# Optimization experiments

Hardware: AMD Instinct MI355X
Metric: run time of the kernel (lower is better)

Reference implementation:

```python
import jax, jax.numpy as jnp
import numpy as np

NUM_HEADS = 32
NUM_KV_HEADS = 8
HEAD_DIM = 128
SCALE = 0.08838834764831845  # 1/sqrt(128)
BATCH = 16
NUM_BLOCKS = 4096
BLOCK_SIZE = 16
BLOCKS_PER_SEQ = 256
MAX_SEQ = BLOCKS_PER_SEQ * BLOCK_SIZE  # 4096


def setup_inputs() -> dict:
    key = jax.random.key(0)
    ks = jax.random.split(key, 8)
    q = jax.random.normal(ks[0], (BATCH, NUM_HEADS, HEAD_DIM), dtype=jnp.float32)
    k = jax.random.normal(ks[1], (BATCH, NUM_KV_HEADS, HEAD_DIM), dtype=jnp.float32)
    v = jax.random.normal(ks[2], (BATCH, NUM_KV_HEADS, HEAD_DIM), dtype=jnp.float32)
    k_cache = jax.random.normal(ks[3], (NUM_BLOCKS, BLOCK_SIZE, NUM_KV_HEADS, HEAD_DIM), dtype=jnp.float32)
    v_cache = jax.random.normal(ks[4], (NUM_BLOCKS, BLOCK_SIZE, NUM_KV_HEADS, HEAD_DIM), dtype=jnp.float32)
    block_tables = jax.random.randint(ks[5], (BATCH, BLOCKS_PER_SEQ), 0, NUM_BLOCKS, dtype=jnp.int32)
    context_lens = jax.random.randint(ks[6], (BATCH,), 1, MAX_SEQ, dtype=jnp.int32)
    slot_mapping = jax.random.randint(ks[7], (BATCH,), 0, NUM_BLOCKS * BLOCK_SIZE, dtype=jnp.int32)
    return {"q": q, "k": k, "v": v, "k_cache": k_cache, "v_cache": v_cache,
            "block_tables": block_tables, "context_lens": context_lens,
            "slot_mapping": slot_mapping}


def reference(q, k, v, k_cache, v_cache, block_tables, context_lens, slot_mapping):
    B = q.shape[0]
    n_rep = NUM_HEADS // NUM_KV_HEADS

    # store_kvcache: scatter new K/V tokens into the flat-slot view of the cache
    kc = k_cache.reshape(-1, NUM_KV_HEADS, HEAD_DIM).at[slot_mapping].set(k)
    vc = v_cache.reshape(-1, NUM_KV_HEADS, HEAD_DIM).at[slot_mapping].set(v)
    kc = kc.reshape(k_cache.shape)
    vc = vc.reshape(v_cache.shape)

    # paged gather: [B, nb, bs, KV, D] -> [B, S, KV, D]
    k_seq = kc[block_tables].reshape(B, -1, NUM_KV_HEADS, HEAD_DIM)
    v_seq = vc[block_tables].reshape(B, -1, NUM_KV_HEADS, HEAD_DIM)
    S = k_seq.shape[1]

    # GQA: group query heads instead of materializing repeat_kv (same math)
    qg = q.reshape(B, NUM_KV_HEADS, n_rep, HEAD_DIM)
    scores = jnp.einsum('bgrd,bsgd->bgrs', qg, k_seq) * SCALE  # [B, KV, n_rep, S]

    valid = jnp.arange(S, dtype=jnp.int32)[None, :] < context_lens[:, None]  # [B, S]
    scores = jnp.where(valid[:, None, None, :], scores, -jnp.inf)
    p = jax.nn.softmax(scores, axis=-1)

    o = jnp.einsum('bgrs,bsgd->bgrd', p, v_seq)  # [B, KV, n_rep, D]
    return o.reshape(B, NUM_HEADS, HEAD_DIM)
```

## Files before the change

### kernel.cpp

```cpp
#include <hip/hip_runtime.h>
#include <math.h>

#define BATCH 16
#define NH 32
#define KVH 8
#define NREP 4
#define HD 128
#define BS 16
#define BPS 256
#define MAXSEQ 4096
#define CHUNK 512
#define CBLK (CHUNK / BS)
#define ATT_SCALE 0.08838834764831845f
#define REC (NREP * HD + 2 * NREP)

__global__ __launch_bounds__(256) void kv_scatter(
    const float* __restrict__ k, const float* __restrict__ v,
    const int* __restrict__ slot_mapping,
    float* __restrict__ k_cache, float* __restrict__ v_cache) {
  int b = blockIdx.x;
  int slot = slot_mapping[b];
  size_t base = (size_t)slot * (KVH * HD);
  for (int i = threadIdx.x; i < KVH * HD; i += 256) {
    k_cache[base + i] = k[b * KVH * HD + i];
    v_cache[base + i] = v[b * KVH * HD + i];
  }
}

__global__ __launch_bounds__(256) void attn_decode(
    const float* __restrict__ q,
    const float* __restrict__ k_cache,
    const float* __restrict__ v_cache,
    const int* __restrict__ block_tables,
    const int* __restrict__ context_lens,
    float* __restrict__ part,
    float* __restrict__ out,
    int nsplits) {
  const int split = blockIdx.x;
  const int kvh   = blockIdx.y;
  const int b     = blockIdx.z;
  const int tid   = threadIdx.x;
  const int ctx   = context_lens[b];
  const int span  = MAXSEQ / nsplits;
  const int s_begin = split * span;

  float* rec = part + (((size_t)b * KVH + kvh) * nsplits + split) * REC;

  if (s_begin >= ctx) {
    if (nsplits > 1 && tid < NREP) {
      rec[NREP * HD + tid] = -INFINITY;
      rec[NREP * HD + NREP + tid] = 0.f;
    }
    return;
  }
  const int s_end = min(ctx, s_begin + span);

  __shared__ float sc[NREP][CHUNK];
  __shared__ int   btab[CBLK];
  __shared__ float red[8][NREP * HD];
  __shared__ float m_sh[NREP], l_sh[NREP], alpha_sh[NREP];

  const int wave = tid >> 6;
  const int lane = tid & 63;
  const int half = lane >> 5;
  const int l32  = lane & 31;
  const int grp  = tid >> 5;
  const int gl   = tid & 31;

  float4 q4[NREP];
#pragma unroll
  for (int h = 0; h < NREP; ++h)
    q4[h] = *(const float4*)(q + ((size_t)b * NH + kvh * NREP + h) * HD + l32 * 4);

  if (tid < NREP) { m_sh[tid] = -INFINITY; l_sh[tid] = 0.f; }

  float acc[NREP][4];
#pragma unroll
  for (int h = 0; h < NREP; ++h)
#pragma unroll
    for (int j = 0; j < 4; ++j) acc[h][j] = 0.f;

  for (int c0 = s_begin; c0 < s_end; c0 += CHUNK) {
    const int n_tok = min(s_end - c0, CHUNK);

    __syncthreads();
    if (tid < CBLK) {
      int bi = (c0 >> 4) + tid;
      btab[tid] = (bi < BPS) ? block_tables[b * BPS + bi] : 0;
    }
    __syncthreads();

    for (int t = wave * 2 + half; t < n_tok; t += 8) {
      int blk = btab[t >> 4];
      const float4 kk = *(const float4*)(
          k_cache + ((size_t)blk * BS + (t & 15)) * (KVH * HD) + kvh * HD + l32 * 4);
      float p0 = kk.x * q4[0].x + kk.y * q4[0].y + kk.z * q4[0].z + kk.w * q4[0].w;
      float p1 = kk.x * q4[1].x + kk.y * q4[1].y + kk.z * q4[1].z + kk.w * q4[1].w;
      float p2 = kk.x * q4[2].x + kk.y * q4[2].y + kk.z * q4[2].z + kk.w * q4[2].w;
      float p3 = kk.x * q4[3].x + kk.y * q4[3].y + kk.z * q4[3].z + kk.w * q4[3].w;
#pragma unroll
      for (int off = 1; off < 32; off <<= 1) {
        p0 += __shfl_xor(p0, off);
        p1 += __shfl_xor(p1, off);
        p2 += __shfl_xor(p2, off);
        p3 += __shfl_xor(p3, off);
      }
      if (l32 == 0) {
        sc[0][t] = p0 * ATT_SCALE;
        sc[1][t] = p1 * ATT_SCALE;
        sc[2][t] = p2 * ATT_SCALE;
        sc[3][t] = p3 * ATT_SCALE;
      }
    }
    __syncthreads();

    {
      const int h = wave;
      float mloc = -INFINITY;
      for (int t = lane; t < n_tok; t += 64) mloc = fmaxf(mloc, sc[h][t]);
#pragma unroll
      for (int off = 1; off < 64; off <<= 1) mloc = fmaxf(mloc, __shfl_xor(mloc, off));
      float m_old = m_sh[h];
      float m_new = fmaxf(m_old, mloc);
      float sum = 0.f;
      for (int t = lane; t < n_tok; t += 64) {
        float e = __expf(sc[h][t] - m_new);
        sc[h][t] = e;
        sum += e;
      }
#pragma unroll
      for (int off = 1; off < 64; off <<= 1) sum += __shfl_xor(sum, off);
      if (lane == 0) {
        float alpha = (m_old == -INFINITY) ? 0.f : __expf(m_old - m_new);
        alpha_sh[h] = alpha;
        l_sh[h] = l_sh[h] * alpha + sum;
        m_sh[h] = m_new;
      }
    }
    __syncthreads();

    {
      float a[NREP] = {alpha_sh[0], alpha_sh[1], alpha_sh[2], alpha_sh[3]};
#pragma unroll
      for (int h = 0; h < NREP; ++h)
#pragma unroll
        for (int j = 0; j < 4; ++j) acc[h][j] *= a[h];
      for (int t = grp; t < n_tok; t += 8) {
        int blk = btab[t >> 4];
        const float4 vv = *(const float4*)(
            v_cache + ((size_t)blk * BS + (t & 15)) * (KVH * HD) + kvh * HD + gl * 4);
#pragma unroll
        for (int h = 0; h < NREP; ++h) {
          float pp = sc[h][t];
          acc[h][0] += pp * vv.x;
          acc[h][1] += pp * vv.y;
          acc[h][2] += pp * vv.z;
          acc[h][3] += pp * vv.w;
        }
      }
    }
  }

#pragma unroll
  for (int h = 0; h < NREP; ++h)
#pragma unroll
    for (int j = 0; j < 4; ++j) red[grp][h * HD + gl * 4 + j] = acc[h][j];
  __syncthreads();

  for (int o = tid; o < NREP * HD; o += 256) {
    float s = 0.f;
#pragma unroll
    for (int g = 0; g < 8; ++g) s += red[g][o];
    int h = o >> 7, d = o & 127;
    if (nsplits == 1) {
      out[((size_t)b * NH + kvh * NREP + h) * HD + d] = s / l_sh[h];
    } else {
      rec[o] = s;
    }
  }
  if (nsplits > 1 && tid < NREP) {
    rec[NREP * HD + tid] = m_sh[tid];
    rec[NREP * HD + NREP + tid] = l_sh[tid];
  }
}

__global__ __launch_bounds__(256) void attn_combine(
    const float* __restrict__ part, float* __restrict__ out, int nsplits) {
  const int kvh = blockIdx.x;
  const int b   = blockIdx.y;
  const int tid = threadIdx.x;
  const float* base = part + ((size_t)b * KVH + kvh) * nsplits * REC;

  __shared__ float w_sh[8][NREP];
  __shared__ float L_sh[NREP];

  if (tid < NREP) {
    const int h = tid;
    float M = -INFINITY;
    for (int s = 0; s < nsplits; ++s)
      M = fmaxf(M, base[s * REC + NREP * HD + h]);
    float L = 0.f;
    for (int s = 0; s < nsplits; ++s) {
      float m = base[s * REC + NREP * HD + h];
      float l = base[s * REC + NREP * HD + NREP + h];
      float w = (l > 0.f) ? __expf(m - M) : 0.f;
      w_sh[s][h] = w;
      L += l * w;
    }
    L_sh[h] = L;
  }
  __syncthreads();

  for (int o = tid; o < NREP * HD; o += 256) {
    int h = o >> 7, d = o & 127;
    float s = 0.f;
    for (int sp = 0; sp < nsplits; ++sp) {
      float w = w_sh[sp][h];
      if (w > 0.f) s += w * base[sp * REC + o];
    }
    out[((size_t)b * NH + kvh * NREP + h) * HD + d] = s / L_sh[h];
  }
}

extern "C" void kernel_launch(void* const* d_in, const int* in_sizes, int n_in,
                              void* d_out, int out_size, void* d_ws, size_t ws_size,
                              hipStream_t stream) {
  const float* q = (const float*)d_in[0];
  const float* k = (const float*)d_in[1];
  const float* v = (const float*)d_in[2];
  float* k_cache = (float*)d_in[3];
  float* v_cache = (float*)d_in[4];
  const int* block_tables = (const int*)d_in[5];
  const int* context_lens = (const int*)d_in[6];
  const int* slot_mapping = (const int*)d_in[7];
  float* out  = (float*)d_out;
  float* part = (float*)d_ws;

  kv_scatter<<<BATCH, 256, 0, stream>>>(k, v, slot_mapping, k_cache, v_cache);

  int nsplits = 8;
  while (nsplits > 1 &&
         (size_t)BATCH * KVH * nsplits * REC * sizeof(float) > ws_size)
    nsplits >>= 1;

  dim3 grid(nsplits, KVH, BATCH);
  attn_decode<<<grid, 256, 0, stream>>>(q, k_cache, v_cache, block_tables,
                                        context_lens, part, out, nsplits);
  if (nsplits > 1)
    attn_combine<<<dim3(KVH, BATCH), 256, 0, stream>>>(part, out, nsplits);
}
```

Before: 526.7 us.

## Stage K tiles in LDS, compute scores per-lane, raise split count to 32

The decode kernel now loads each 64-token K chunk into a padded shared-memory tile. Each lane computes a full token score from that tile, which replaces the per-token 32-lane shuffle reductions, and softmax state lives in registers per wave. The split-K count rises from 8 to 32, giving many more workgroups, which is meant to improve occupancy and memory-level parallelism for this small batch. The scatter kernel is vectorised to float4. The cost is more chunk iterations with extra barriers, and more partial records for the combine kernel to read.

```diff
diff --git a/kernel.cpp b/kernel.cpp
--- a/kernel.cpp
+++ b/kernel.cpp
@@ -9,8 +9,9 @@
 #define BS 16
 #define BPS 256
 #define MAXSEQ 4096
-#define CHUNK 512
-#define CBLK (CHUNK / BS)
+#define NSPLIT_MAX 32
+#define CH 64
+#define KT_STRIDE 33
 #define ATT_SCALE 0.08838834764831845f
 #define REC (NREP * HD + 2 * NREP)
 
@@ -20,11 +21,10 @@
     float* __restrict__ k_cache, float* __restrict__ v_cache) {
   int b = blockIdx.x;
   int slot = slot_mapping[b];
-  size_t base = (size_t)slot * (KVH * HD);
-  for (int i = threadIdx.x; i < KVH * HD; i += 256) {
-    k_cache[base + i] = k[b * KVH * HD + i];
-    v_cache[base + i] = v[b * KVH * HD + i];
-  }
+  size_t base = (size_t)slot * (KVH * HD) + threadIdx.x * 4;
+  size_t src = (size_t)b * (KVH * HD) + threadIdx.x * 4;
+  *(float4*)(k_cache + base) = *(const float4*)(k + src);
+  *(float4*)(v_cache + base) = *(const float4*)(v + src);
 }
 
 __global__ __launch_bounds__(256) void attn_decode(
@@ -55,100 +55,92 @@
   }
   const int s_end = min(ctx, s_begin + span);
 
-  __shared__ float sc[NREP][CHUNK];
-  __shared__ int   btab[CBLK];
-  __shared__ float red[8][NREP * HD];
-  __shared__ float m_sh[NREP], l_sh[NREP], alpha_sh[NREP];
+  __shared__ float4 kt[CH * KT_STRIDE];
+  __shared__ float4 sq[NREP * 32];
+  __shared__ float  sc[NREP][CH];
+  __shared__ int    btab[CH / BS];
+  __shared__ float  alpha_sh[NREP], l_sh[NREP];
 
   const int wave = tid >> 6;
   const int lane = tid & 63;
-  const int half = lane >> 5;
-  const int l32  = lane & 31;
   const int grp  = tid >> 5;
   const int gl   = tid & 31;
 
-  float4 q4[NREP];
+  if (tid < NREP * 32)
+    sq[tid] = *(const float4*)(
+        q + ((size_t)b * NH + kvh * NREP + (tid >> 5)) * HD + (tid & 31) * 4);
+
+  float m_w = -INFINITY, l_w = 0.f;
+  float acc[NREP][4];
 #pragma unroll
   for (int h = 0; h < NREP; ++h)
-    q4[h] = *(const float4*)(q + ((size_t)b * NH + kvh * NREP + h) * HD + l32 * 4);
-
-  if (tid < NREP) { m_sh[tid] = -INFINITY; l_sh[tid] = 0.f; }
-
-  float acc[NREP][4];
-#pragma unroll
-  for (int h = 0; h < NREP; ++h)
 #pragma unroll
     for (int j = 0; j < 4; ++j) acc[h][j] = 0.f;
 
-  for (int c0 = s_begin; c0 < s_end; c0 += CHUNK) {
-    const int n_tok = min(s_end - c0, CHUNK);
-
-    __syncthreads();
-    if (tid < CBLK) {
-      int bi = (c0 >> 4) + tid;
-      btab[tid] = (bi < BPS) ? block_tables[b * BPS + bi] : 0;
-    }
-    __syncthreads();
-
-    for (int t = wave * 2 + half; t < n_tok; t += 8) {
-      int blk = btab[t >> 4];
-      const float4 kk = *(const float4*)(
-          k_cache + ((size_t)blk * BS + (t & 15)) * (KVH * HD) + kvh * HD + l32 * 4);
-      float p0 = kk.x * q4[0].x + kk.y * q4[0].y + kk.z * q4[0].z + kk.w * q4[0].w;
-      float p1 = kk.x * q4[1].x + kk.y * q4[1].y + kk.z * q4[1].z + kk.w * q4[1].w;
-      float p2 = kk.x * q4[2].x + kk.y * q4[2].y + kk.z * q4[2].z + kk.w * q4[2].w;
-      float p3 = kk.x * q4[3].x + kk.y * q4[3].y + kk.z * q4[3].z + kk.w * q4[3].w;
-#pragma unroll
-      for (int off = 1; off < 32; off <<= 1) {
-        p0 += __shfl_xor(p0, off);
-        p1 += __shfl_xor(p1, off);
-        p2 += __shfl_xor(p2, off);
-        p3 += __shfl_xor(p3, off);
-      }
-      if (l32 == 0) {
-        sc[0][t] = p0 * ATT_SCALE;
-        sc[1][t] = p1 * ATT_SCALE;
-        sc[2][t] = p2 * ATT_SCALE;
-        sc[3][t] = p3 * ATT_SCALE;
-      }
-    }
+  const size_t head_off = (size_t)kvh * HD;
+
+  for (int c0 = s_begin; c0 < s_end; c0 += CH) {
+    const int n_tok = min(s_end - c0, CH);
+
+    __syncthreads();
+    if (tid < CH / BS) btab[tid] = block_tables[b * BPS + (c0 >> 4) + tid];
     __syncthreads();
 
     {
-      const int h = wave;
-      float mloc = -INFINITY;
-      for (int t = lane; t < n_tok; t += 64) mloc = fmaxf(mloc, sc[h][t]);
-#pragma unroll
-      for (int off = 1; off < 64; off <<= 1) mloc = fmaxf(mloc, __shfl_xor(mloc, off));
-      float m_old = m_sh[h];
-      float m_new = fmaxf(m_old, mloc);
-      float sum = 0.f;
-      for (int t = lane; t < n_tok; t += 64) {
-        float e = __expf(sc[h][t] - m_new);
-        sc[h][t] = e;
-        sum += e;
-      }
+      const int c = tid & 31;
+      int r = tid >> 5;
+#pragma unroll
+      for (int i = 0; i < CH / 8; ++i, r += 8) {
+        int blk = btab[r >> 4];
+        kt[r * KT_STRIDE + c] = *(const float4*)(
+            k_cache + ((size_t)blk * BS + (r & 15)) * (KVH * HD) + head_off + c * 4);
+      }
+    }
+    __syncthreads();
+
+    {
+      const int t = lane;
+      const float4* krow = &kt[t * KT_STRIDE];
+      const float4* qh = &sq[wave * 32];
+      float4 ps = {0.f, 0.f, 0.f, 0.f};
+#pragma unroll 8
+      for (int c = 0; c < 32; ++c) {
+        float4 kk = krow[c];
+        float4 qq = qh[c];
+        ps.x += kk.x * qq.x;
+        ps.y += kk.y * qq.y;
+        ps.z += kk.z * qq.z;
+        ps.w += kk.w * qq.w;
+      }
+      const bool valid = t < n_tok;
+      float s = (ps.x + ps.y + ps.z + ps.w) * ATT_SCALE;
+      float mloc = valid ? s : -INFINITY;
+#pragma unroll
+      for (int off = 1; off < 64; off <<= 1)
+        mloc = fmaxf(mloc, __shfl_xor(mloc, off));
+      float m_new = fmaxf(m_w, mloc);
+      float e = valid ? __expf(s - m_new) : 0.f;
+      float sum = e;
 #pragma unroll
       for (int off = 1; off < 64; off <<= 1) sum += __shfl_xor(sum, off);
-      if (lane == 0) {
-        float alpha = (m_old == -INFINITY) ? 0.f : __expf(m_old - m_new);
-        alpha_sh[h] = alpha;
-        l_sh[h] = l_sh[h] * alpha + sum;
-        m_sh[h] = m_new;
-      }
+      float alpha = (m_w == -INFINITY) ? 0.f : __expf(m_w - m_new);
+      l_w = l_w * alpha + sum;
+      m_w = m_new;
+      sc[wave][t] = e;
+      if (lane == 0) alpha_sh[wave] = alpha;
     }
     __syncthreads();
 
     {
-      float a[NREP] = {alpha_sh[0], alpha_sh[1], alpha_sh[2], alpha_sh[3]};
-#pragma unroll
-      for (int h = 0; h < NREP; ++h)
-#pragma unroll
-        for (int j = 0; j < 4; ++j) acc[h][j] *= a[h];
+      float a0 = alpha_sh[0], a1 = alpha_sh[1], a2 = alpha_sh[2], a3 = alpha_sh[3];
+#pragma unroll
+      for (int j = 0; j < 4; ++j) {
+        acc[0][j] *= a0; acc[1][j] *= a1; acc[2][j] *= a2; acc[3][j] *= a3;
+      }
       for (int t = grp; t < n_tok; t += 8) {
         int blk = btab[t >> 4];
         const float4 vv = *(const float4*)(
-            v_cache + ((size_t)blk * BS + (t & 15)) * (KVH * HD) + kvh * HD + gl * 4);
+            v_cache + ((size_t)blk * BS + (t & 15)) * (KVH * HD) + head_off + gl * 4);
 #pragma unroll
         for (int h = 0; h < NREP; ++h) {
           float pp = sc[h][t];
@@ -161,26 +153,31 @@
     }
   }
 
+  if (lane == 0) {
+    l_sh[wave] = l_w;
+    if (nsplits > 1) {
+      rec[NREP * HD + wave] = m_w;
+      rec[NREP * HD + NREP + wave] = l_w;
+    }
+  }
+  float* red = (float*)kt;
 #pragma unroll
   for (int h = 0; h < NREP; ++h)
 #pragma unroll
-    for (int j = 0; j < 4; ++j) red[grp][h * HD + gl * 4 + j] = acc[h][j];
+    for (int j = 0; j < 4; ++j)
+      red[(grp * NREP + h) * HD + gl * 4 + j] = acc[h][j];
   __syncthreads();
 
   for (int o = tid; o < NREP * HD; o += 256) {
     float s = 0.f;
 #pragma unroll
-    for (int g = 0; g < 8; ++g) s += red[g][o];
+    for (int g = 0; g < 8; ++g) s += red[(g * NREP) * HD + o];
     int h = o >> 7, d = o & 127;
     if (nsplits == 1) {
       out[((size_t)b * NH + kvh * NREP + h) * HD + d] = s / l_sh[h];
     } else {
       rec[o] = s;
     }
-  }
-  if (nsplits > 1 && tid < NREP) {
-    rec[NREP * HD + tid] = m_sh[tid];
-    rec[NREP * HD + NREP + tid] = l_sh[tid];
   }
 }
 
@@ -191,7 +188,7 @@
   const int tid = threadIdx.x;
   const float* base = part + ((size_t)b * KVH + kvh) * nsplits * REC;
 
-  __shared__ float w_sh[8][NREP];
+  __shared__ float w_sh[NSPLIT_MAX][NREP];
   __shared__ float L_sh[NREP];
 
   if (tid < NREP) {
@@ -238,7 +235,7 @@
 
   kv_scatter<<<BATCH, 256, 0, stream>>>(k, v, slot_mapping, k_cache, v_cache);
 
-  int nsplits = 8;
+  int nsplits = NSPLIT_MAX;
   while (nsplits > 1 &&
          (size_t)BATCH * KVH * nsplits * REC * sizeof(float) > ws_size)
     nsplits >>= 1;
```

Result: faster. 505.7 us (-4.0%).
